# Optimization experiments

Measured on AMD Instinct MI355X. Metric: run time of the kernel, lower is better.

## Reference

```python
import jax, jax.numpy as jnp
import numpy as np

B, T, D, H = 2, 2048, 1024, 16
DH = D // H

def setup_inputs() -> dict:
    key = jax.random.key(0)
    k1, k2, k3 = jax.random.split(key, 3)
    x = jax.random.normal(k1, (B, T, D), dtype=jnp.float32)
    Wqkv = jax.random.normal(k2, (D, 3 * D), dtype=jnp.float32) * (1.0 / np.sqrt(D))
    Wo = jax.random.normal(k3, (D, D), dtype=jnp.float32) * (1.0 / np.sqrt(D))
    return {"x": x, "Wqkv": Wqkv, "Wo": Wo}

def reference(x, Wqkv, Wo):
    b, t, d = x.shape
    qkv = x @ Wqkv                      # [B,T,3D]
    q, k, v = jnp.split(qkv, 3, axis=-1)
    q = q.reshape(b, t, H, DH)          # [B,T,H,DH]
    k = k.reshape(b, t, H, DH)
    v = v.reshape(b, t, H, DH)
    scale = 1.0 / np.sqrt(DH).astype(np.float32)
    scores = jnp.einsum('bqhd,bkhd->bhqk', q, k) * scale  # [B,H,T,T]
    causal = jnp.tril(jnp.ones((t, t), dtype=bool))       # True = keep
    scores = jnp.where(causal, scores, jnp.finfo(scores.dtype).min)
    attn = jax.nn.softmax(scores, axis=-1)
    y = jnp.einsum('bhqk,bkhd->bqhd', attn, v)            # [B,T,H,DH]
    y = y.reshape(b, t, d)
    return y @ Wo
```

## Files before the change

kernel.cpp:

```cpp
#include <hip/hip_runtime.h>
#include <stdint.h>

typedef __attribute__((ext_vector_type(8))) short short8;
typedef __attribute__((ext_vector_type(8))) __bf16 bf16x8;
typedef __attribute__((ext_vector_type(4))) float f32x4;
typedef __attribute__((ext_vector_type(2))) unsigned int u32x2;

#define T_SEQ 2048

static __device__ __forceinline__ ushort f2bf(float f) {
  uint32_t u = __float_as_uint(f);
  u += 0x7fffu + ((u >> 16) & 1u);
  return (ushort)(u >> 16);
}

static __device__ __forceinline__ uint32_t cvtpk(float lo, float hi) {
  uint32_t r;
  asm("v_cvt_pk_bf16_f32 %0, %1, %2" : "=v"(r) : "v"(lo), "v"(hi));
  return r;
}

static __device__ __forceinline__ f32x4 mfma16(short8 a, short8 b, f32x4 c) {
  return __builtin_amdgcn_mfma_f32_16x16x32_bf16(
      __builtin_bit_cast(bf16x8, a), __builtin_bit_cast(bf16x8, b), c, 0, 0, 0);
}

static __device__ __forceinline__ void gload16(const ushort* g, char* l) {
  __builtin_amdgcn_global_load_lds(
      (const __attribute__((address_space(1))) void*)g,
      (__attribute__((address_space(3))) void*)l, 16, 0, 0);
}

__global__ __launch_bounds__(256) void cvt_bf16_k(const float* __restrict__ in,
                                                  ushort* __restrict__ out) {
  int i = (blockIdx.x * 256 + threadIdx.x) * 8;
  float4 a = *(const float4*)(in + i);
  float4 b = *(const float4*)(in + i + 4);
  short8 o;
  ((ushort*)&o)[0] = f2bf(a.x); ((ushort*)&o)[1] = f2bf(a.y);
  ((ushort*)&o)[2] = f2bf(a.z); ((ushort*)&o)[3] = f2bf(a.w);
  ((ushort*)&o)[4] = f2bf(b.x); ((ushort*)&o)[5] = f2bf(b.y);
  ((ushort*)&o)[6] = f2bf(b.z); ((ushort*)&o)[7] = f2bf(b.w);
  *(short8*)(out + i) = o;
}

__global__ __launch_bounds__(256) void transpose_cvt2_k(
    const float* __restrict__ Wqkv, const float* __restrict__ Wo,
    ushort* __restrict__ WqkvT, ushort* __restrict__ WoT) {
  __shared__ ushort t[64][65];
  const int K = 1024;
  const float* in;
  ushort* out;
  int N, byl;
  if (blockIdx.y < 48) { in = Wqkv; out = WqkvT; N = 3072; byl = blockIdx.y; }
  else                 { in = Wo;   out = WoT;   N = 1024; byl = blockIdx.y - 48; }
  const int bk = blockIdx.x * 64, bn = byl * 64;
  const int r = threadIdx.x >> 2, c0 = (threadIdx.x & 3) << 4;
  const float* src = in + (size_t)(bk + r) * N + bn + c0;
#pragma unroll
  for (int q = 0; q < 4; ++q) {
    float4 a = *(const float4*)(src + q * 4);
    t[r][c0 + q * 4 + 0] = f2bf(a.x);
    t[r][c0 + q * 4 + 1] = f2bf(a.y);
    t[r][c0 + q * 4 + 2] = f2bf(a.z);
    t[r][c0 + q * 4 + 3] = f2bf(a.w);
  }
  __syncthreads();
  short8 o0, o1;
#pragma unroll
  for (int j = 0; j < 8; ++j) {
    ((ushort*)&o0)[j] = t[c0 + j][r];
    ((ushort*)&o1)[j] = t[c0 + 8 + j][r];
  }
  ushort* dst = out + (size_t)(bn + r) * K + bk + c0;
  *(short8*)(dst) = o0;
  *(short8*)(dst + 8) = o1;
}

__global__ __launch_bounds__(512) void gemm256(const ushort* __restrict__ A,
                                               const ushort* __restrict__ Bt,
                                               ushort* __restrict__ C,
                                               int Ndim) {
  __shared__ char sA[2][32768];
  __shared__ char sB[2][32768];
  const int tid = threadIdx.x;
  const int lane = tid & 63, wid = tid >> 6;
  const int wm = wid >> 2, wn = wid & 3;
  const int lc = lane & 15, lg = lane >> 4;
  const int bm = blockIdx.x * 256, bn = blockIdx.y * 256;
  const int lane16 = lane << 4;

  f32x4 acc[8][4] = {};

#define STAGE256(tt, bb)                                                   \
  do {                                                                     \
    _Pragma("unroll") for (int i_ = 0; i_ < 4; ++i_) {                     \
      int v_ = tid + i_ * 512;                                             \
      int row_ = v_ >> 3;                                                  \
      int cbl_ = (v_ & 7) << 4;                                            \
      int ce_ = (cbl_ ^ ((row_ & 7) << 4)) >> 1;                           \
      char* la_ = sA[bb] + ((v_ << 4) - lane16);                           \
      char* lb_ = sB[bb] + ((v_ << 4) - lane16);                           \
      gload16(A + (size_t)(bm + row_) * 1024 + (tt) * 64 + ce_, la_);      \
      gload16(Bt + (size_t)(bn + row_) * 1024 + (tt) * 64 + ce_, lb_);     \
    }                                                                      \
  } while (0)

  STAGE256(0, 0);
  STAGE256(1, 1);

  for (int t = 0; t < 16; ++t) {
    const int cur = t & 1;
    if (t < 15) asm volatile("s_waitcnt vmcnt(8)" ::: "memory");
    else        asm volatile("s_waitcnt vmcnt(0)" ::: "memory");
    __builtin_amdgcn_s_barrier();
    __builtin_amdgcn_sched_barrier(0);
#pragma unroll
    for (int ks = 0; ks < 2; ++ks) {
      const int kb = ks * 64 + lg * 16;
      short8 bf[4];
#pragma unroll
      for (int nf = 0; nf < 4; ++nf) {
        int row = wn * 64 + nf * 16 + lc;
        bf[nf] = *(const short8*)&sB[cur][(row << 7) + (kb ^ ((row & 7) << 4))];
      }
#pragma unroll
      for (int mh = 0; mh < 2; ++mh) {
        short8 af[4];
#pragma unroll
        for (int mf = 0; mf < 4; ++mf) {
          int row = wm * 128 + mh * 64 + mf * 16 + lc;
          af[mf] = *(const short8*)&sA[cur][(row << 7) + (kb ^ ((row & 7) << 4))];
        }
        __builtin_amdgcn_s_setprio(1);
#pragma unroll
        for (int mf = 0; mf < 4; ++mf)
#pragma unroll
          for (int nf = 0; nf < 4; ++nf)
            acc[mh * 4 + mf][nf] = mfma16(af[mf], bf[nf], acc[mh * 4 + mf][nf]);
        __builtin_amdgcn_s_setprio(0);
      }
    }
    asm volatile("s_waitcnt lgkmcnt(0)" ::: "memory");
    __builtin_amdgcn_sched_barrier(0);
    __builtin_amdgcn_s_barrier();
    __builtin_amdgcn_sched_barrier(0);
    if (t + 2 < 16) STAGE256(t + 2, cur);
  }
#undef STAGE256

#pragma unroll
  for (int mf = 0; mf < 8; ++mf) {
    int rowb = bm + wm * 128 + mf * 16 + lg * 4;
#pragma unroll
    for (int nf = 0; nf < 4; ++nf) {
      int col = bn + wn * 64 + nf * 16 + lc;
#pragma unroll
      for (int r = 0; r < 4; ++r)
        C[(size_t)(rowb + r) * Ndim + col] = f2bf(acc[mf][nf][r]);
    }
  }
}

__global__ __launch_bounds__(256) void gemm128p(const ushort* __restrict__ A,
                                                const ushort* __restrict__ Bt,
                                                void* __restrict__ Cv,
                                                int Ndim, int Kdim, int f32out) {
  __shared__ char sA[2][16384];
  __shared__ char sB[2][16384];
  const int tid = threadIdx.x;
  const int lane = tid & 63, wid = tid >> 6;
  const int wm = wid >> 1, wn = wid & 1;
  const int lc = lane & 15, lg = lane >> 4;
  const int bm = blockIdx.x * 128, bn = blockIdx.y * 128;
  const int lane16 = lane << 4;
  const int nk = Kdim >> 6;

  f32x4 acc[4][4] = {};

#define STAGE128(tt, bb)                                                   \
  do {                                                                     \
    _Pragma("unroll") for (int i_ = 0; i_ < 4; ++i_) {                     \
      int v_ = tid + i_ * 256;                                             \
      int row_ = v_ >> 3;                                                  \
      int cbl_ = (v_ & 7) << 4;                                            \
      int ce_ = (cbl_ ^ ((row_ & 7) << 4)) >> 1;                           \
      char* la_ = sA[bb] + ((v_ << 4) - lane16);                           \
      char* lb_ = sB[bb] + ((v_ << 4) - lane16);                           \
      gload16(A + (size_t)(bm + row_) * Kdim + (tt) * 64 + ce_, la_);      \
      gload16(Bt + (size_t)(bn + row_) * Kdim + (tt) * 64 + ce_, lb_);     \
    }                                                                      \
  } while (0)

  STAGE128(0, 0);
  STAGE128(1, 1);

  for (int t = 0; t < nk; ++t) {
    const int cur = t & 1;
    if (t < nk - 1) asm volatile("s_waitcnt vmcnt(8)" ::: "memory");
    else            asm volatile("s_waitcnt vmcnt(0)" ::: "memory");
    __builtin_amdgcn_s_barrier();
    __builtin_amdgcn_sched_barrier(0);
#pragma unroll
    for (int ks = 0; ks < 2; ++ks) {
      const int kb = ks * 64 + lg * 16;
      short8 af[4], bfr[4];
#pragma unroll
      for (int m = 0; m < 4; ++m) {
        int row = wm * 64 + m * 16 + lc;
        af[m] = *(const short8*)&sA[cur][(row << 7) + (kb ^ ((row & 7) << 4))];
      }
#pragma unroll
      for (int n = 0; n < 4; ++n) {
        int row = wn * 64 + n * 16 + lc;
        bfr[n] = *(const short8*)&sB[cur][(row << 7) + (kb ^ ((row & 7) << 4))];
      }
      __builtin_amdgcn_s_setprio(1);
#pragma unroll
      for (int m = 0; m < 4; ++m)
#pragma unroll
        for (int n = 0; n < 4; ++n)
          acc[m][n] = mfma16(af[m], bfr[n], acc[m][n]);
      __builtin_amdgcn_s_setprio(0);
    }
    asm volatile("s_waitcnt lgkmcnt(0)" ::: "memory");
    __builtin_amdgcn_sched_barrier(0);
    __builtin_amdgcn_s_barrier();
    __builtin_amdgcn_sched_barrier(0);
    if (t + 2 < nk) STAGE128(t + 2, cur);
  }
#undef STAGE128

#pragma unroll
  for (int m = 0; m < 4; ++m) {
    int rowb = bm + wm * 64 + m * 16 + lg * 4;
#pragma unroll
    for (int n = 0; n < 4; ++n) {
      int col = bn + wn * 64 + n * 16 + lc;
      if (f32out) {
        float* C = (float*)Cv;
#pragma unroll
        for (int r = 0; r < 4; ++r)
          C[(size_t)(rowb + r) * Ndim + col] = acc[m][n][r];
      } else {
        ushort* C = (ushort*)Cv;
#pragma unroll
        for (int r = 0; r < 4; ++r)
          C[(size_t)(rowb + r) * Ndim + col] = f2bf(acc[m][n][r]);
      }
    }
  }
}

__global__ __launch_bounds__(512) void attn_k(const ushort* __restrict__ qkv,
                                              ushort* __restrict__ Y) {
  __shared__ char sK[8192];
  __shared__ char sV[8192];
  __shared__ char sP[16384];
  __shared__ float sL[8][16];
  const int tid = threadIdx.x;
  const int lane = tid & 63, wid = tid >> 6;
  const int lc = lane & 15, lg = lane >> 4;
  const int orig = blockIdx.x;
  const int xcd = orig & 7, slot = orig >> 3;
  int tile, bhl;
  if (slot < 32) { tile = slot >> 2;              bhl = slot & 3; }
  else           { tile = 15 - ((slot - 32) >> 2); bhl = (slot - 32) & 3; }
  const int bh = xcd * 4 + bhl;
  const int b = bh >> 4, h = bh & 15;
  char* sPw = sP + (wid << 11);

  const ushort* base = qkv + (size_t)b * T_SEQ * 3072 + h * 64;
  const int q0 = tile * 128 + wid * 16;

  const int kt = tid >> 3, kce = (tid & 7) << 3, kcb = kce << 1;
  const int ksw = (kt & 7) << 4;
  const int vt = tid & 63, vd0 = (tid >> 6) << 3;
  const ushort* kbase = base + 1024;
  const ushort* vbase = base + 2048;

  short8 qf[2];
#pragma unroll
  for (int ks = 0; ks < 2; ++ks)
    qf[ks] = *(const short8*)(base + (size_t)(q0 + lc) * 3072 + ks * 32 + lg * 8);

  f32x4 o[4] = {};
  float lsum = 0.f;

  const float cexp = 0.125f * 1.4426950408889634f;
  const int nkb = 2 * (tile + 1);
  const int qmaxw = q0 + 15;

  short8 kr = *(const short8*)(kbase + (size_t)kt * 3072 + kce);
  short8 vr = *(const short8*)(vbase + (size_t)vt * 3072 + vd0);

  for (int kb = 0; kb < nkb; ++kb) {
    __syncthreads();
    *(short8*)&sK[(kt << 7) + (kcb ^ ksw)] = kr;
#pragma unroll
    for (int j = 0; j < 8; ++j) {
      int d = vd0 + j;
      *(ushort*)&sV[(d << 7) + ((2 * vt) ^ ((d & 7) << 4))] = ((const ushort*)&vr)[j];
    }
    __syncthreads();
    if (kb + 1 < nkb) {
      kr = *(const short8*)(kbase + (size_t)((kb + 1) * 64 + kt) * 3072 + kce);
      vr = *(const short8*)(vbase + (size_t)((kb + 1) * 64 + vt) * 3072 + vd0);
    }
    if (kb * 64 > qmaxw) continue;

    f32x4 S[4] = {};
    __builtin_amdgcn_s_setprio(1);
#pragma unroll
    for (int ks = 0; ks < 2; ++ks) {
      int kbyt = ks * 64 + lg * 16;
      short8 kf[4];
#pragma unroll
      for (int n = 0; n < 4; ++n) {
        int row = n * 16 + lc;
        kf[n] = *(const short8*)&sK[(row << 7) + (kbyt ^ ((row & 7) << 4))];
      }
#pragma unroll
      for (int n = 0; n < 4; ++n)
        S[n] = mfma16(kf[n], qf[ks], S[n]);
    }
    __builtin_amdgcn_s_setprio(0);

    const bool diag = (kb * 64 + 63 > q0);
    {
      int q = q0 + lc;
      float lacc = 0.f;
#pragma unroll
      for (int n = 0; n < 4; ++n) {
        int kg = kb * 64 + n * 16 + lg * 4;
        f32x4 pe;
#pragma unroll
        for (int r = 0; r < 4; ++r) {
          pe[r] = exp2f(S[n][r] * cexp);
          if (diag && (kg + r > q)) pe[r] = 0.f;
        }
        lacc += (pe[0] + pe[1]) + (pe[2] + pe[3]);
        u32x2 w;
        w[0] = cvtpk(pe[0], pe[1]);
        w[1] = cvtpk(pe[2], pe[3]);
        int colb = n * 32 + lg * 8;
        *(u32x2*)&sPw[(lc << 7) + (colb ^ ((lc & 7) << 4))] = w;
      }
      lsum += lacc;
    }
    asm volatile("" ::: "memory");
    __builtin_amdgcn_s_setprio(1);
#pragma unroll
    for (int ks = 0; ks < 2; ++ks) {
      int kbyt = ks * 64 + lg * 16;
      short8 pf = *(const short8*)&sPw[(lc << 7) + (kbyt ^ ((lc & 7) << 4))];
      short8 vf[4];
#pragma unroll
      for (int dn = 0; dn < 4; ++dn) {
        int row = dn * 16 + lc;
        vf[dn] = *(const short8*)&sV[(row << 7) + (kbyt ^ ((row & 7) << 4))];
      }
#pragma unroll
      for (int dn = 0; dn < 4; ++dn)
        o[dn] = mfma16(pf, vf[dn], o[dn]);
    }
    __builtin_amdgcn_s_setprio(0);
  }
  {
    float v = lsum;
    v += __shfl_xor(v, 16);
    v += __shfl_xor(v, 32);
    sL[wid][lc] = 1.0f / v;
  }
  asm volatile("" ::: "memory");
  {
    float lr[4];
#pragma unroll
    for (int r = 0; r < 4; ++r) lr[r] = sL[wid][lg * 4 + r];
#pragma unroll
    for (int dn = 0; dn < 4; ++dn) {
#pragma unroll
      for (int r = 0; r < 4; ++r) {
        int t = q0 + lg * 4 + r;
        Y[(size_t)(b * T_SEQ + t) * 1024 + h * 64 + dn * 16 + lc] =
            f2bf(o[dn][r] * lr[r]);
      }
    }
  }
}

extern "C" void kernel_launch(void* const* d_in, const int* in_sizes, int n_in,
                              void* d_out, int out_size, void* d_ws, size_t ws_size,
                              hipStream_t stream) {
  const float* x    = (const float*)d_in[0];
  const float* Wqkv = (const float*)d_in[1];
  const float* Wo   = (const float*)d_in[2];
  for (int i = 0; i < n_in; ++i) {
    if (in_sizes[i] == 4194304) x = (const float*)d_in[i];
    else if (in_sizes[i] == 3145728) Wqkv = (const float*)d_in[i];
    else if (in_sizes[i] == 1048576) Wo = (const float*)d_in[i];
  }
  float* out = (float*)d_out;

  ushort* xb    = (ushort*)d_ws;
  ushort* WqkvT = xb + (size_t)4096 * 1024;
  ushort* WoT   = WqkvT + (size_t)3072 * 1024;
  ushort* QKV   = WoT + (size_t)1024 * 1024;
  ushort* Yb    = QKV + (size_t)4096 * 3072;

  cvt_bf16_k<<<2048, 256, 0, stream>>>(x, xb);
  transpose_cvt2_k<<<dim3(16, 64), 256, 0, stream>>>(Wqkv, Wo, WqkvT, WoT);
  gemm256<<<dim3(16, 12), 512, 0, stream>>>(xb, WqkvT, QKV, 3072);
  attn_k<<<512, 512, 0, stream>>>(QKV, Yb);
  gemm128p<<<dim3(32, 8), 256, 0, stream>>>(Yb, WoT, out, 1024, 1024, 1);
}
```

Baseline: 117.4 us.

## Retile QKV GEMM to 256x192 blocks and merge prep kernels into one launch

The QKV projection GEMM now uses 256x192 output tiles with 6 waves (2x3), instead of 256x256 tiles with 8 waves. That raises the grid from 192 to 256 blocks, so every CU on a 256-CU device gets work instead of leaving a quarter idle. The global-to-LDS staging loop is rewritten for the uneven A/B chunk counts, and the vmcnt wait is adjusted to match. The fp32-to-bf16 conversion of x and the weight transpose-convert kernels are merged into a single launch to save one kernel launch. The trade-off is fewer waves per block, and a less regular load distribution in which some threads issue one extra load.

```diff
diff --git a/kernel.cpp b/kernel.cpp
--- a/kernel.cpp
+++ b/kernel.cpp
@@ -31,30 +31,33 @@
       (__attribute__((address_space(3))) void*)l, 16, 0, 0);
 }
 
-__global__ __launch_bounds__(256) void cvt_bf16_k(const float* __restrict__ in,
-                                                  ushort* __restrict__ out) {
-  int i = (blockIdx.x * 256 + threadIdx.x) * 8;
-  float4 a = *(const float4*)(in + i);
-  float4 b = *(const float4*)(in + i + 4);
-  short8 o;
-  ((ushort*)&o)[0] = f2bf(a.x); ((ushort*)&o)[1] = f2bf(a.y);
-  ((ushort*)&o)[2] = f2bf(a.z); ((ushort*)&o)[3] = f2bf(a.w);
-  ((ushort*)&o)[4] = f2bf(b.x); ((ushort*)&o)[5] = f2bf(b.y);
-  ((ushort*)&o)[6] = f2bf(b.z); ((ushort*)&o)[7] = f2bf(b.w);
-  *(short8*)(out + i) = o;
-}
-
-__global__ __launch_bounds__(256) void transpose_cvt2_k(
-    const float* __restrict__ Wqkv, const float* __restrict__ Wo,
-    ushort* __restrict__ WqkvT, ushort* __restrict__ WoT) {
+__global__ __launch_bounds__(256) void prep_k(const float* __restrict__ x,
+                                              const float* __restrict__ Wqkv,
+                                              const float* __restrict__ Wo,
+                                              ushort* __restrict__ xb,
+                                              ushort* __restrict__ WqkvT,
+                                              ushort* __restrict__ WoT) {
+  if (blockIdx.x < 2048) {
+    int i = (blockIdx.x * 256 + threadIdx.x) * 8;
+    float4 a = *(const float4*)(x + i);
+    float4 b = *(const float4*)(x + i + 4);
+    short8 o;
+    ((ushort*)&o)[0] = f2bf(a.x); ((ushort*)&o)[1] = f2bf(a.y);
+    ((ushort*)&o)[2] = f2bf(a.z); ((ushort*)&o)[3] = f2bf(a.w);
+    ((ushort*)&o)[4] = f2bf(b.x); ((ushort*)&o)[5] = f2bf(b.y);
+    ((ushort*)&o)[6] = f2bf(b.z); ((ushort*)&o)[7] = f2bf(b.w);
+    *(short8*)(xb + i) = o;
+    return;
+  }
   __shared__ ushort t[64][65];
-  const int K = 1024;
+  int tb = blockIdx.x - 2048;
   const float* in;
   ushort* out;
   int N, byl;
-  if (blockIdx.y < 48) { in = Wqkv; out = WqkvT; N = 3072; byl = blockIdx.y; }
-  else                 { in = Wo;   out = WoT;   N = 1024; byl = blockIdx.y - 48; }
-  const int bk = blockIdx.x * 64, bn = byl * 64;
+  if (tb < 768) { in = Wqkv; out = WqkvT; N = 3072; byl = tb >> 4; }
+  else          { in = Wo;   out = WoT;   N = 1024; byl = (tb - 768) >> 4; }
+  const int K = 1024;
+  const int bk = (tb & 15) * 64, bn = byl * 64;
   const int r = threadIdx.x >> 2, c0 = (threadIdx.x & 3) << 4;
   const float* src = in + (size_t)(bk + r) * N + bn + c0;
 #pragma unroll
@@ -77,41 +80,50 @@
   *(short8*)(dst + 8) = o1;
 }
 
-__global__ __launch_bounds__(512) void gemm256(const ushort* __restrict__ A,
+__global__ __launch_bounds__(384) void gemm192(const ushort* __restrict__ A,
                                                const ushort* __restrict__ Bt,
                                                ushort* __restrict__ C,
                                                int Ndim) {
   __shared__ char sA[2][32768];
-  __shared__ char sB[2][32768];
+  __shared__ char sB[2][24576];
   const int tid = threadIdx.x;
   const int lane = tid & 63, wid = tid >> 6;
-  const int wm = wid >> 2, wn = wid & 3;
+  const int wm = (wid >= 3) ? 1 : 0, wn = wid - wm * 3;
   const int lc = lane & 15, lg = lane >> 4;
-  const int bm = blockIdx.x * 256, bn = blockIdx.y * 256;
+  const int bm = blockIdx.x * 256, bn = blockIdx.y * 192;
   const int lane16 = lane << 4;
 
   f32x4 acc[8][4] = {};
 
-#define STAGE256(tt, bb)                                                   \
-  do {                                                                     \
-    _Pragma("unroll") for (int i_ = 0; i_ < 4; ++i_) {                     \
-      int v_ = tid + i_ * 512;                                             \
-      int row_ = v_ >> 3;                                                  \
-      int cbl_ = (v_ & 7) << 4;                                            \
-      int ce_ = (cbl_ ^ ((row_ & 7) << 4)) >> 1;                           \
-      char* la_ = sA[bb] + ((v_ << 4) - lane16);                           \
-      char* lb_ = sB[bb] + ((v_ << 4) - lane16);                           \
-      gload16(A + (size_t)(bm + row_) * 1024 + (tt) * 64 + ce_, la_);      \
-      gload16(Bt + (size_t)(bn + row_) * 1024 + (tt) * 64 + ce_, lb_);     \
-    }                                                                      \
+#define STAGE192(tt, bb)                                                    \
+  do {                                                                      \
+    _Pragma("unroll") for (int i_ = 0; i_ < 10; ++i_) {                     \
+      int c_ = tid + i_ * 384;                                              \
+      if (c_ < 3584) {                                                      \
+        if (c_ < 2048) {                                                    \
+          int row_ = c_ >> 3;                                               \
+          int cbl_ = (c_ & 7) << 4;                                         \
+          int ce_ = (cbl_ ^ ((row_ & 7) << 4)) >> 1;                        \
+          gload16(A + (size_t)(bm + row_) * 1024 + (tt) * 64 + ce_,         \
+                  sA[bb] + ((c_ << 4) - lane16));                           \
+        } else {                                                            \
+          int c2_ = c_ - 2048;                                              \
+          int row_ = c2_ >> 3;                                              \
+          int cbl_ = (c2_ & 7) << 4;                                        \
+          int ce_ = (cbl_ ^ ((row_ & 7) << 4)) >> 1;                        \
+          gload16(Bt + (size_t)(bn + row_) * 1024 + (tt) * 64 + ce_,        \
+                  sB[bb] + ((c2_ << 4) - lane16));                          \
+        }                                                                   \
+      }                                                                     \
+    }                                                                       \
   } while (0)
 
-  STAGE256(0, 0);
-  STAGE256(1, 1);
+  STAGE192(0, 0);
+  STAGE192(1, 1);
 
   for (int t = 0; t < 16; ++t) {
     const int cur = t & 1;
-    if (t < 15) asm volatile("s_waitcnt vmcnt(8)" ::: "memory");
+    if (t < 15) asm volatile("s_waitcnt vmcnt(9)" ::: "memory");
     else        asm volatile("s_waitcnt vmcnt(0)" ::: "memory");
     __builtin_amdgcn_s_barrier();
     __builtin_amdgcn_sched_barrier(0);
@@ -145,9 +157,9 @@
     __builtin_amdgcn_sched_barrier(0);
     __builtin_amdgcn_s_barrier();
     __builtin_amdgcn_sched_barrier(0);
-    if (t + 2 < 16) STAGE256(t + 2, cur);
-  }
-#undef STAGE256
+    if (t + 2 < 16) STAGE192(t + 2, cur);
+  }
+#undef STAGE192
 
 #pragma unroll
   for (int mf = 0; mf < 8; ++mf) {
@@ -408,9 +420,8 @@
   ushort* QKV   = WoT + (size_t)1024 * 1024;
   ushort* Yb    = QKV + (size_t)4096 * 3072;
 
-  cvt_bf16_k<<<2048, 256, 0, stream>>>(x, xb);
-  transpose_cvt2_k<<<dim3(16, 64), 256, 0, stream>>>(Wqkv, Wo, WqkvT, WoT);
-  gemm256<<<dim3(16, 12), 512, 0, stream>>>(xb, WqkvT, QKV, 3072);
+  prep_k<<<3072, 256, 0, stream>>>(x, Wqkv, Wo, xb, WqkvT, WoT);
+  gemm192<<<dim3(16, 16), 384, 0, stream>>>(xb, WqkvT, QKV, 3072);
   attn_k<<<512, 512, 0, stream>>>(QKV, Yb);
   gemm128p<<<dim3(32, 8), 256, 0, stream>>>(Yb, WoT, out, 1024, 1024, 1);
 }
```

Measured after the change: 117.7 us. No clear change (+0.2%).
